# Performance work log

Measured on AMD Instinct MI355X. Metric: run time of the kernel, lower is better.

Reference implementation:

```python
import jax, jax.numpy as jnp
import numpy as np

B, S, D, H = 2, 2048, 1024, 16
DK = D // H  # 64


def setup_inputs() -> dict:
    key = jax.random.key(0)
    ks = jax.random.split(key, 5)
    query_input = jax.random.normal(ks[0], (B, S, D), dtype=jnp.float32)
    # additive mask: 1.0 where attention is disallowed (causal upper triangle)
    mask = jnp.triu(jnp.ones((S, S), dtype=jnp.float32), k=1)[None, None, :, :]
    scale = 1.0 / np.sqrt(D)
    wq = jax.random.normal(ks[1], (D, D), dtype=jnp.float32) * scale
    wk = jax.random.normal(ks[2], (D, D), dtype=jnp.float32) * scale
    wv = jax.random.normal(ks[3], (D, D), dtype=jnp.float32) * scale
    wo = jax.random.normal(ks[4], (D, D), dtype=jnp.float32) * scale
    return {"query_input": query_input, "mask": mask, "wq": wq, "wk": wk, "wv": wv, "wo": wo}


def _split_heads(x):
    # [B, S, D] -> [B, H, S, DK]
    b, s, _ = x.shape
    return x.reshape(b, s, H, DK).transpose(0, 2, 1, 3)


def reference(query_input, mask, wq, wk, wv, wo):
    # self-attention: key_input = value_input = query_input
    q = _split_heads(query_input @ wq)  # [B, H, S, DK]
    k = _split_heads(query_input @ wk)
    v = _split_heads(query_input @ wv)
    scores = jnp.einsum('bhqd,bhkd->bhqk', q, k) / jnp.sqrt(jnp.float32(DK))
    scores = scores + mask * (-1e9)
    attn = jax.nn.softmax(scores, axis=-1)
    out = jnp.einsum('bhqk,bhkd->bhqd', attn, v)  # [B, H, S, DK]
    out = out.transpose(0, 2, 1, 3).reshape(query_input.shape[0], -1, D)
    return out @ wo
```

## Files before the change

### kernel.cpp

```cpp
#include <hip/hip_runtime.h>

typedef __attribute__((ext_vector_type(8))) short bf16x8;
typedef __attribute__((ext_vector_type(4))) float f32x4;
typedef __attribute__((ext_vector_type(4))) unsigned short u16x4;

#define S_LEN 2048
#define D_DIM 1024
#define NHEAD 16
#define DK 64
#define BH 32
#define MROWS 4096

__device__ __forceinline__ unsigned short f2bf(float f) {
    unsigned int u = __float_as_uint(f);
    u += 0x7fffu + ((u >> 16) & 1u);
    return (unsigned short)(u >> 16);
}

__device__ __forceinline__ unsigned int pk_bf16(float a, float b) {
    unsigned int r;
    asm("v_cvt_pk_bf16_f32 %0, %1, %2" : "=v"(r) : "v"(a), "v"(b));
    return r;
}

__device__ __forceinline__ void gload16(const void* g, void* l) {
    __builtin_amdgcn_global_load_lds(
        (const __attribute__((address_space(1))) void*)g,
        (__attribute__((address_space(3))) void*)l, 16, 0, 0);
}

__global__ __launch_bounds__(256) void cast_x_kernel(const float* __restrict__ X,
                                                     unsigned short* __restrict__ Xb) {
    int idx = blockIdx.x * 256 + threadIdx.x;
    float4 v = ((const float4*)X)[idx];
    u16x4 o;
    o.x = f2bf(v.x); o.y = f2bf(v.y); o.z = f2bf(v.z); o.w = f2bf(v.w);
    ((u16x4*)Xb)[idx] = o;
}

__global__ __launch_bounds__(256) void wtrans_kernel(const float* __restrict__ wq,
                                                     const float* __restrict__ wk,
                                                     const float* __restrict__ wv,
                                                     const float* __restrict__ wo,
                                                     unsigned short* __restrict__ Wt) {
    int z = blockIdx.z;
    const float* W = (z == 0) ? wq : (z == 1) ? wk : (z == 2) ? wv : wo;
    unsigned short* O = Wt + (size_t)z * D_DIM * D_DIM;
    __shared__ float t[32][33];
    int tx = threadIdx.x, ty = threadIdx.y;
    int bx = blockIdx.x * 32;
    int by = blockIdx.y * 32;
#pragma unroll
    for (int i = 0; i < 4; ++i)
        t[ty + i * 8][tx] = W[(size_t)(by + ty + i * 8) * D_DIM + bx + tx];
    __syncthreads();
#pragma unroll
    for (int i = 0; i < 4; ++i)
        O[(size_t)(bx + ty + i * 8) * D_DIM + by + tx] = f2bf(t[tx][ty + i * 8]);
}

__device__ __forceinline__ void gemm_mainloop(const unsigned short* __restrict__ A,
                                              const unsigned short* __restrict__ Bt,
                                              int K, int m0, int n0,
                                              unsigned short* As, unsigned short* Bs,
                                              f32x4 acc[4][4]) {
    const int tid = threadIdx.x;
    const int lane = tid & 63, wid = tid >> 6;
    const int wr = wid >> 1, wc = wid & 1;
    const int fr = lane & 15, fk = (lane >> 4) * 8;
    for (int k0 = 0; k0 < K; k0 += 32) {
        __syncthreads();
#pragma unroll
        for (int c = 0; c < 2; ++c) {
            int idx = c * 256 + tid;
            int row = idx >> 2;
            int col = (idx & 3) * 8;
            int base = (c * 256 + wid * 64) * 8;
            gload16(&A[(size_t)(m0 + row) * K + k0 + col], &As[base]);
            gload16(&Bt[(size_t)(n0 + row) * K + k0 + col], &Bs[base]);
        }
        __syncthreads();
        bf16x8 af[4], bfr[4];
#pragma unroll
        for (int i = 0; i < 4; ++i)
            af[i] = *(const bf16x8*)&As[(wr * 64 + i * 16 + fr) * 32 + fk];
#pragma unroll
        for (int j = 0; j < 4; ++j)
            bfr[j] = *(const bf16x8*)&Bs[(wc * 64 + j * 16 + fr) * 32 + fk];
#pragma unroll
        for (int i = 0; i < 4; ++i)
#pragma unroll
            for (int j = 0; j < 4; ++j)
                acc[i][j] = __builtin_amdgcn_mfma_f32_16x16x32_bf16(af[i], bfr[j], acc[i][j], 0, 0, 0);
    }
}

#define QSCALE 0.18033688011112042f
__global__ __launch_bounds__(256) void gemm_qkv_kernel(const unsigned short* __restrict__ Xb,
                                                       const unsigned short* __restrict__ Wt,
                                                       unsigned short* __restrict__ QKV) {
    __shared__ __align__(16) unsigned short As[128 * 32];
    __shared__ __align__(16) unsigned short Bs[128 * 32];
    const unsigned short* Bt = Wt + (size_t)blockIdx.z * D_DIM * D_DIM;
    unsigned short* Out = QKV + (size_t)blockIdx.z * MROWS * D_DIM;
    int m0 = blockIdx.y * 128, n0 = blockIdx.x * 128;
    f32x4 acc[4][4] = {};
    gemm_mainloop(Xb, Bt, D_DIM, m0, n0, As, Bs, acc);
    const float qs = (blockIdx.z == 0) ? QSCALE : 1.0f;
    const int lane = threadIdx.x & 63, wid = threadIdx.x >> 6;
    const int wr = wid >> 1, wc = wid & 1;
#pragma unroll
    for (int i = 0; i < 4; ++i)
#pragma unroll
        for (int j = 0; j < 4; ++j)
#pragma unroll
            for (int r = 0; r < 4; ++r) {
                int gm = m0 + wr * 64 + i * 16 + (lane >> 4) * 4 + r;
                int gn = n0 + wc * 64 + j * 16 + (lane & 15);
                int b = gm >> 11, s = gm & 2047, h = gn >> 6, dk = gn & 63;
                Out[((size_t)((b * NHEAD + h) * S_LEN + s)) * DK + dk] = f2bf(acc[i][j][r] * qs);
            }
}

__global__ __launch_bounds__(256) void vtrans_kernel(const unsigned short* __restrict__ V,
                                                     unsigned short* __restrict__ Vt) {
    __shared__ unsigned short tile[64][65];
    int bh = blockIdx.y;
    int s0 = blockIdx.x * 64;
    int t = threadIdx.x;
#pragma unroll
    for (int i = 0; i < 16; ++i) {
        int idx = i * 256 + t;
        int row = idx >> 6, col = idx & 63;
        tile[row][col] = V[((size_t)bh * S_LEN + s0 + row) * DK + col];
    }
    __syncthreads();
#pragma unroll
    for (int i = 0; i < 16; ++i) {
        int idx = i * 256 + t;
        int dr = idx >> 6, sc = idx & 63;
        Vt[((size_t)bh * DK + dr) * S_LEN + s0 + sc] = tile[sc][dr];
    }
}

__global__ __launch_bounds__(256) void attn_kernel(const unsigned short* __restrict__ QKV,
                                                   const unsigned short* __restrict__ Vt,
                                                   unsigned short* __restrict__ AO) {
    const int bh = blockIdx.x;
    const int qi = 31 - (int)blockIdx.y;
    const int tid = threadIdx.x, lane = tid & 63, wid = tid >> 6;
    const int fr = lane & 15, fkg = lane >> 4, fk = fkg * 8;
    const unsigned short* Q = QKV;
    const unsigned short* Kd = QKV + (size_t)MROWS * D_DIM;

    __shared__ __align__(16) unsigned short Ks[2][64][64];
    __shared__ __align__(16) unsigned short Vs[2][64][64];
    __shared__ __align__(16) unsigned short Ps[4][16][64];

    const int b = bh >> 4, h = bh & 15;
    const int rsw  = fr & 7;
    const int off0 = (fkg ^ rsw) * 8;
    const int off1 = ((4 + fkg) ^ rsw) * 8;

    const int q0 = qi * 64;
    const int qr = q0 + wid * 16;

    bf16x8 qf0 = *(const bf16x8*)&Q[((size_t)bh * S_LEN + qr + fr) * DK + fk];
    bf16x8 qf1 = *(const bf16x8*)&Q[((size_t)bh * S_LEN + qr + fr) * DK + 32 + fk];

    f32x4 o[4] = {};
    float m = -1e30f, l = 0.f;
    const int ntiles = qi + 1;
    int buf = 0;

#pragma unroll
    for (int c = 0; c < 2; ++c) {
        int chunk = wid * 128 + c * 64 + lane;
        int row = chunk >> 3;
        int scol = ((chunk & 7) ^ (row & 7)) * 8;
        int base = (wid * 128 + c * 64) * 8;
        gload16(&Kd[((size_t)bh * S_LEN + row) * DK + scol], &Ks[0][0][0] + base);
        gload16(&Vt[((size_t)bh * DK + row) * S_LEN + scol], &Vs[0][0][0] + base);
    }
    __syncthreads();

    for (int t = 0; t < ntiles; ++t) {
        if (t + 1 < ntiles) {
            const int ktn = (t + 1) * 64;
#pragma unroll
            for (int c = 0; c < 2; ++c) {
                int chunk = wid * 128 + c * 64 + lane;
                int row = chunk >> 3;
                int scol = ((chunk & 7) ^ (row & 7)) * 8;
                int base = (wid * 128 + c * 64) * 8;
                gload16(&Kd[((size_t)bh * S_LEN + ktn + row) * DK + scol], &Ks[buf ^ 1][0][0] + base);
                gload16(&Vt[((size_t)bh * DK + row) * S_LEN + ktn + scol], &Vs[buf ^ 1][0][0] + base);
            }
        }

        f32x4 s4[4];
#pragma unroll
        for (int nj = 0; nj < 4; ++nj) {
            const unsigned short* krow = &Ks[buf][nj * 16 + fr][0];
            bf16x8 kf0 = *(const bf16x8*)&krow[off0];
            bf16x8 kf1 = *(const bf16x8*)&krow[off1];
            f32x4 z = {};
            z = __builtin_amdgcn_mfma_f32_16x16x32_bf16(kf0, qf0, z, 0, 0, 0);
            z = __builtin_amdgcn_mfma_f32_16x16x32_bf16(kf1, qf1, z, 0, 0, 0);
            s4[nj] = z;
        }

        if (t == ntiles - 1) {
            const int qoff = wid * 16 + fr;
#pragma unroll
            for (int nj = 0; nj < 4; ++nj)
#pragma unroll
                for (int r = 0; r < 4; ++r)
                    s4[nj][r] = (nj * 16 + fkg * 4 + r > qoff) ? -1e30f : s4[nj][r];
        }

        float m0_ = fmaxf(fmaxf(s4[0][0], s4[0][1]), fmaxf(s4[0][2], s4[0][3]));
        float m1_ = fmaxf(fmaxf(s4[1][0], s4[1][1]), fmaxf(s4[1][2], s4[1][3]));
        float m2_ = fmaxf(fmaxf(s4[2][0], s4[2][1]), fmaxf(s4[2][2], s4[2][3]));
        float m3_ = fmaxf(fmaxf(s4[3][0], s4[3][1]), fmaxf(s4[3][2], s4[3][3]));
        float mt = fmaxf(fmaxf(m0_, m1_), fmaxf(m2_, m3_));
        mt = fmaxf(mt, __shfl_xor(mt, 16, 64));
        mt = fmaxf(mt, __shfl_xor(mt, 32, 64));
        if (!__all(mt <= m + 8.0f)) {
            float mn = fmaxf(m, mt);
            float corr = exp2f(m - mn);
            m = mn;
            l *= corr;
            o[0] *= corr; o[1] *= corr; o[2] *= corr; o[3] *= corr;
        }
        float ps = 0.f;
        unsigned int pw[4][2];
#pragma unroll
        for (int nj = 0; nj < 4; ++nj) {
            float p0 = exp2f(s4[nj][0] - m);
            float p1 = exp2f(s4[nj][1] - m);
            float p2 = exp2f(s4[nj][2] - m);
            float p3 = exp2f(s4[nj][3] - m);
            ps += (p0 + p1) + (p2 + p3);
            pw[nj][0] = pk_bf16(p0, p1);
            pw[nj][1] = pk_bf16(p2, p3);
        }
        ps += __shfl_xor(ps, 16, 64);
        ps += __shfl_xor(ps, 32, 64);
        l += ps;

#pragma unroll
        for (int nj = 0; nj < 4; ++nj) {
            int chunk = nj * 2 + (fkg >> 1);
            int el = (fkg & 1) * 4;
            *(uint2*)&Ps[wid][fr][((chunk ^ rsw) << 3) + el] = make_uint2(pw[nj][0], pw[nj][1]);
        }
        bf16x8 pf0 = *(const bf16x8*)&Ps[wid][fr][off0];
        bf16x8 pf1 = *(const bf16x8*)&Ps[wid][fr][off1];
#pragma unroll
        for (int j = 0; j < 4; ++j) {
            const unsigned short* vrow = &Vs[buf][j * 16 + fr][0];
            bf16x8 vf0 = *(const bf16x8*)&vrow[off0];
            bf16x8 vf1 = *(const bf16x8*)&vrow[off1];
            o[j] = __builtin_amdgcn_mfma_f32_16x16x32_bf16(vf0, pf0, o[j], 0, 0, 0);
            o[j] = __builtin_amdgcn_mfma_f32_16x16x32_bf16(vf1, pf1, o[j], 0, 0, 0);
        }

        __syncthreads();
        buf ^= 1;
    }

    float inv = 1.0f / l;
    size_t rowoff = ((size_t)(b * S_LEN) + qr + fr) * D_DIM + h * DK;
#pragma unroll
    for (int j = 0; j < 4; ++j) {
        u16x4 w;
        w.x = f2bf(o[j][0] * inv); w.y = f2bf(o[j][1] * inv);
        w.z = f2bf(o[j][2] * inv); w.w = f2bf(o[j][3] * inv);
        *(u16x4*)&AO[rowoff + j * 16 + fkg * 4] = w;
    }
}

__global__ __launch_bounds__(256) void gemm_out_kernel(const unsigned short* __restrict__ AO,
                                                       const unsigned short* __restrict__ Wot,
                                                       float* __restrict__ out) {
    __shared__ __align__(16) unsigned short As[128 * 32];
    __shared__ __align__(16) unsigned short Bs[128 * 32];
    int m0 = blockIdx.y * 128, n0 = blockIdx.x * 128;
    f32x4 acc[4][4] = {};
    gemm_mainloop(AO, Wot, D_DIM, m0, n0, As, Bs, acc);
    const int lane = threadIdx.x & 63, wid = threadIdx.x >> 6;
    const int wr = wid >> 1, wc = wid & 1;
#pragma unroll
    for (int i = 0; i < 4; ++i)
#pragma unroll
        for (int j = 0; j < 4; ++j)
#pragma unroll
            for (int r = 0; r < 4; ++r) {
                int gm = m0 + wr * 64 + i * 16 + (lane >> 4) * 4 + r;
                int gn = n0 + wc * 64 + j * 16 + (lane & 15);
                out[(size_t)gm * D_DIM + gn] = acc[i][j][r];
            }
}

extern "C" void kernel_launch(void* const* d_in, const int* in_sizes, int n_in,
                              void* d_out, int out_size, void* d_ws, size_t ws_size,
                              hipStream_t stream) {
    (void)in_sizes; (void)n_in; (void)out_size; (void)ws_size;
    const float* X  = (const float*)d_in[0];
    const float* wq = (const float*)d_in[2];
    const float* wk = (const float*)d_in[3];
    const float* wv = (const float*)d_in[4];
    const float* wo = (const float*)d_in[5];

    char* ws = (char*)d_ws;
    unsigned short* Xb  = (unsigned short*)(ws);
    unsigned short* Wt  = (unsigned short*)(ws + ((size_t)8  << 20));
    unsigned short* QKV = (unsigned short*)(ws + ((size_t)16 << 20));
    unsigned short* Vt  = (unsigned short*)(ws + ((size_t)40 << 20));
    unsigned short* AO  = (unsigned short*)(ws + ((size_t)48 << 20));
    float* out = (float*)d_out;

    cast_x_kernel<<<4096, 256, 0, stream>>>(X, Xb);
    wtrans_kernel<<<dim3(32, 32, 4), dim3(32, 8), 0, stream>>>(wq, wk, wv, wo, Wt);
    gemm_qkv_kernel<<<dim3(8, 32, 3), 256, 0, stream>>>(Xb, Wt, QKV);
    vtrans_kernel<<<dim3(32, 32), 256, 0, stream>>>(QKV + (size_t)2 * MROWS * D_DIM, Vt);
    attn_kernel<<<dim3(32, 32), 256, 0, stream>>>(QKV, Vt, AO);
    gemm_out_kernel<<<dim3(8, 32), 256, 0, stream>>>(AO, Wt + (size_t)3 * D_DIM * D_DIM, out);
}
```

Baseline: 123.0 us.

## Use 128-row query tiles with 8 waves and keep QKV in row-major layout

The attention kernel now runs 512 threads (8 waves) over a 128-row query block, so each K/V tile loaded into shared memory is shared by twice as many query rows and the grid is halved. The QKV GEMM now writes a plain [M, D] row-major layout instead of head-split scatter stores, and the attention and V-transpose kernels index per head with a D_DIM stride. MFMA sections are wrapped in s_setprio to favour matrix work across waves. The causal mask is now applied per wave based on row offset. Risks include lower occupancy from the larger blocks, more wasted work on the diagonal tiles, and strided per-head reads.

```diff
diff --git a/kernel.cpp b/kernel.cpp
--- a/kernel.cpp
+++ b/kernel.cpp
@@ -117,8 +117,7 @@
             for (int r = 0; r < 4; ++r) {
                 int gm = m0 + wr * 64 + i * 16 + (lane >> 4) * 4 + r;
                 int gn = n0 + wc * 64 + j * 16 + (lane & 15);
-                int b = gm >> 11, s = gm & 2047, h = gn >> 6, dk = gn & 63;
-                Out[((size_t)((b * NHEAD + h) * S_LEN + s)) * DK + dk] = f2bf(acc[i][j][r] * qs);
+                Out[(size_t)gm * D_DIM + gn] = f2bf(acc[i][j][r] * qs);
             }
 }
 
@@ -126,13 +125,14 @@
                                                      unsigned short* __restrict__ Vt) {
     __shared__ unsigned short tile[64][65];
     int bh = blockIdx.y;
+    int b = bh >> 4, h = bh & 15;
     int s0 = blockIdx.x * 64;
     int t = threadIdx.x;
 #pragma unroll
     for (int i = 0; i < 16; ++i) {
         int idx = i * 256 + t;
         int row = idx >> 6, col = idx & 63;
-        tile[row][col] = V[((size_t)bh * S_LEN + s0 + row) * DK + col];
+        tile[row][col] = V[((size_t)(b * S_LEN) + s0 + row) * D_DIM + h * DK + col];
     }
     __syncthreads();
 #pragma unroll
@@ -143,11 +143,11 @@
     }
 }
 
-__global__ __launch_bounds__(256) void attn_kernel(const unsigned short* __restrict__ QKV,
-                                                   const unsigned short* __restrict__ Vt,
-                                                   unsigned short* __restrict__ AO) {
+__global__ __launch_bounds__(512, 4) void attn_kernel(const unsigned short* __restrict__ QKV,
+                                                      const unsigned short* __restrict__ Vt,
+                                                      unsigned short* __restrict__ AO) {
     const int bh = blockIdx.x;
-    const int qi = 31 - (int)blockIdx.y;
+    const int qi = 15 - (int)blockIdx.y;
     const int tid = threadIdx.x, lane = tid & 63, wid = tid >> 6;
     const int fr = lane & 15, fkg = lane >> 4, fk = fkg * 8;
     const unsigned short* Q = QKV;
@@ -155,50 +155,43 @@
 
     __shared__ __align__(16) unsigned short Ks[2][64][64];
     __shared__ __align__(16) unsigned short Vs[2][64][64];
-    __shared__ __align__(16) unsigned short Ps[4][16][64];
+    __shared__ __align__(16) unsigned short Ps[8][16][64];
 
     const int b = bh >> 4, h = bh & 15;
     const int rsw  = fr & 7;
     const int off0 = (fkg ^ rsw) * 8;
     const int off1 = ((4 + fkg) ^ rsw) * 8;
 
-    const int q0 = qi * 64;
+    const int srow = tid >> 3;
+    const int scol = ((tid & 7) ^ (srow & 7)) * 8;
+    const int sbase = wid * 512;
+
+    const int q0 = qi * 128;
     const int qr = q0 + wid * 16;
 
-    bf16x8 qf0 = *(const bf16x8*)&Q[((size_t)bh * S_LEN + qr + fr) * DK + fk];
-    bf16x8 qf1 = *(const bf16x8*)&Q[((size_t)bh * S_LEN + qr + fr) * DK + 32 + fk];
+    bf16x8 qf0 = *(const bf16x8*)&Q[((size_t)(b * S_LEN) + qr + fr) * D_DIM + h * DK + fk];
+    bf16x8 qf1 = *(const bf16x8*)&Q[((size_t)(b * S_LEN) + qr + fr) * D_DIM + h * DK + 32 + fk];
 
     f32x4 o[4] = {};
     float m = -1e30f, l = 0.f;
-    const int ntiles = qi + 1;
+    const int ntiles = 2 * qi + 2;
     int buf = 0;
 
-#pragma unroll
-    for (int c = 0; c < 2; ++c) {
-        int chunk = wid * 128 + c * 64 + lane;
-        int row = chunk >> 3;
-        int scol = ((chunk & 7) ^ (row & 7)) * 8;
-        int base = (wid * 128 + c * 64) * 8;
-        gload16(&Kd[((size_t)bh * S_LEN + row) * DK + scol], &Ks[0][0][0] + base);
-        gload16(&Vt[((size_t)bh * DK + row) * S_LEN + scol], &Vs[0][0][0] + base);
-    }
+    gload16(&Kd[((size_t)(b * S_LEN) + srow) * D_DIM + h * DK + scol], &Ks[0][0][0] + sbase);
+    gload16(&Vt[((size_t)bh * DK + srow) * S_LEN + scol], &Vs[0][0][0] + sbase);
     __syncthreads();
 
     for (int t = 0; t < ntiles; ++t) {
         if (t + 1 < ntiles) {
             const int ktn = (t + 1) * 64;
-#pragma unroll
-            for (int c = 0; c < 2; ++c) {
-                int chunk = wid * 128 + c * 64 + lane;
-                int row = chunk >> 3;
-                int scol = ((chunk & 7) ^ (row & 7)) * 8;
-                int base = (wid * 128 + c * 64) * 8;
-                gload16(&Kd[((size_t)bh * S_LEN + ktn + row) * DK + scol], &Ks[buf ^ 1][0][0] + base);
-                gload16(&Vt[((size_t)bh * DK + row) * S_LEN + ktn + scol], &Vs[buf ^ 1][0][0] + base);
-            }
+            gload16(&Kd[((size_t)(b * S_LEN) + ktn + srow) * D_DIM + h * DK + scol],
+                    &Ks[buf ^ 1][0][0] + sbase);
+            gload16(&Vt[((size_t)bh * DK + srow) * S_LEN + ktn + scol],
+                    &Vs[buf ^ 1][0][0] + sbase);
         }
 
         f32x4 s4[4];
+        __builtin_amdgcn_s_setprio(1);
 #pragma unroll
         for (int nj = 0; nj < 4; ++nj) {
             const unsigned short* krow = &Ks[buf][nj * 16 + fr][0];
@@ -209,9 +202,10 @@
             z = __builtin_amdgcn_mfma_f32_16x16x32_bf16(kf1, qf1, z, 0, 0, 0);
             s4[nj] = z;
         }
-
-        if (t == ntiles - 1) {
-            const int qoff = wid * 16 + fr;
+        __builtin_amdgcn_s_setprio(0);
+
+        if (64 * t + 63 > qr) {
+            const int qoff = qr + fr - 64 * t;
 #pragma unroll
             for (int nj = 0; nj < 4; ++nj)
 #pragma unroll
@@ -257,6 +251,7 @@
         }
         bf16x8 pf0 = *(const bf16x8*)&Ps[wid][fr][off0];
         bf16x8 pf1 = *(const bf16x8*)&Ps[wid][fr][off1];
+        __builtin_amdgcn_s_setprio(1);
 #pragma unroll
         for (int j = 0; j < 4; ++j) {
             const unsigned short* vrow = &Vs[buf][j * 16 + fr][0];
@@ -265,6 +260,7 @@
             o[j] = __builtin_amdgcn_mfma_f32_16x16x32_bf16(vf0, pf0, o[j], 0, 0, 0);
             o[j] = __builtin_amdgcn_mfma_f32_16x16x32_bf16(vf1, pf1, o[j], 0, 0, 0);
         }
+        __builtin_amdgcn_s_setprio(0);
 
         __syncthreads();
         buf ^= 1;
@@ -325,6 +321,6 @@
     wtrans_kernel<<<dim3(32, 32, 4), dim3(32, 8), 0, stream>>>(wq, wk, wv, wo, Wt);
     gemm_qkv_kernel<<<dim3(8, 32, 3), 256, 0, stream>>>(Xb, Wt, QKV);
     vtrans_kernel<<<dim3(32, 32), 256, 0, stream>>>(QKV + (size_t)2 * MROWS * D_DIM, Vt);
-    attn_kernel<<<dim3(32, 32), 256, 0, stream>>>(QKV, Vt, AO);
+    attn_kernel<<<dim3(32, 16), 512, 0, stream>>>(QKV, Vt, AO);
     gemm_out_kernel<<<dim3(8, 32), 256, 0, stream>>>(AO, Wt + (size_t)3 * D_DIM * D_DIM, out);
 }
```

Result: no change. 122.3 us (-0.6%).
